# Kernel tuning notes

Measured on AMD Instinct MI355X. Metric: run time of the kernel, lower is better.

Reference implementation:

```python
import jax, jax.numpy as jnp
import numpy as np

N_NODES = 50000
N_EDGES = 640000
N_REL = 8
IN_DIM = 128
HID_DIM = 128
OUT_DIM = 64


def setup_inputs() -> dict:
    key = jax.random.key(0)
    ks = jax.random.split(key, 8)
    features = jax.random.normal(ks[0], (N_NODES, IN_DIM), dtype=jnp.float32)
    src = jax.random.randint(ks[1], (N_EDGES,), 0, N_NODES, dtype=jnp.int32)
    dst = jax.random.randint(ks[2], (N_EDGES,), 0, N_NODES, dtype=jnp.int32)
    edge_types = jax.random.randint(ks[3], (N_EDGES,), 0, N_REL, dtype=jnp.int32)
    s1 = 1.0 / np.sqrt(IN_DIM)
    s2 = 1.0 / np.sqrt(HID_DIM)
    W1 = jax.random.normal(ks[4], (N_REL, IN_DIM, HID_DIM), dtype=jnp.float32) * s1
    W1_self = jax.random.normal(ks[5], (IN_DIM, HID_DIM), dtype=jnp.float32) * s1
    b1 = jnp.zeros((HID_DIM,), dtype=jnp.float32)
    W2 = jax.random.normal(ks[6], (N_REL, HID_DIM, OUT_DIM), dtype=jnp.float32) * s2
    W2_self = jax.random.normal(ks[7], (HID_DIM, OUT_DIM), dtype=jnp.float32) * s2
    b2 = jnp.zeros((OUT_DIM,), dtype=jnp.float32)
    return {"features": features, "src": src, "dst": dst, "edge_types": edge_types,
            "W1": W1, "W1_self": W1_self, "b1": b1,
            "W2": W2, "W2_self": W2_self, "b2": b2}


def _rel_graph_conv(h, src, dst, edge_types, W, W_self, b):
    # Precompute relation-specific transforms for all nodes: [R, N, Dout]
    rel = jnp.einsum('nd,rdo->rno', h, W)
    # Gather per-edge message W[etype(e)] @ h[src(e)]: [E, Dout]
    msg = rel[edge_types, src]
    # Scatter-sum to destination nodes
    agg = jax.ops.segment_sum(msg, dst, num_segments=h.shape[0])
    # Self-loop + bias (DGL RelGraphConv defaults: self_loop=True, bias=True)
    return agg + h @ W_self + b


def reference(features, src, dst, edge_types, W1, W1_self, b1, W2, W2_self, b2):
    h = jax.nn.relu(_rel_graph_conv(features, src, dst, edge_types, W1, W1_self, b1))
    logits = _rel_graph_conv(h, src, dst, edge_types, W2, W2_self, b2)
    return logits
```

## Files before the change

kernel.cpp:

```cpp
#include <hip/hip_runtime.h>
#include <hip/hip_bf16.h>
#include <stdint.h>

#define NN 50000
#define NE 640000
#define NR 8
#define NK (NR * NN)
#define NB2 ((NK + 1023) / 1024)

typedef short bf16x8 __attribute__((ext_vector_type(8)));
typedef float f32x4  __attribute__((ext_vector_type(4)));

__device__ __forceinline__ unsigned short f2bf(float f) {
    union { float f; unsigned u; } v; v.f = f;
    unsigned r = v.u + 0x7FFF + ((v.u >> 16) & 1);
    return (unsigned short)(r >> 16);
}

__global__ void hist2_kernel(const int* __restrict__ dst, const int* __restrict__ et,
                             int* __restrict__ counts) {
    int e = blockIdx.x * 256 + threadIdx.x;
    if (e < NE) atomicAdd(&counts[et[e] * NN + dst[e]], 1);
}

__global__ __launch_bounds__(1024) void blocksum_kernel(const int* __restrict__ counts,
                                                        int* __restrict__ bsum, int n) {
    __shared__ int ws[16];
    int i = blockIdx.x * 1024 + threadIdx.x;
    int v = (i < n) ? counts[i] : 0;
    #pragma unroll
    for (int d = 32; d > 0; d >>= 1) v += __shfl_down(v, d, 64);
    int wid = threadIdx.x >> 6, lane = threadIdx.x & 63;
    if (lane == 0) ws[wid] = v;
    __syncthreads();
    if (threadIdx.x < 16) {
        int s = ws[threadIdx.x];
        #pragma unroll
        for (int d = 8; d > 0; d >>= 1) s += __shfl_down(s, d, 16);
        if (threadIdx.x == 0) bsum[blockIdx.x] = s;
    }
}

__global__ __launch_bounds__(512) void scanbase_kernel(const int* __restrict__ bsum,
                                                       int* __restrict__ base,
                                                       int* __restrict__ total, int nb) {
    __shared__ int ws[8];
    int t = threadIdx.x, lane = t & 63, wid = t >> 6;
    int v = (t < nb) ? bsum[t] : 0;
    int incl = v;
    #pragma unroll
    for (int d = 1; d < 64; d <<= 1) {
        int nv = __shfl_up(incl, d, 64);
        if (lane >= d) incl += nv;
    }
    if (lane == 63) ws[wid] = incl;
    __syncthreads();
    if (t < 8) {
        int s = ws[t], si = s;
        #pragma unroll
        for (int d = 1; d < 8; d <<= 1) {
            int nv = __shfl_up(si, d, 8);
            if (t >= d) si += nv;
        }
        ws[t] = si - s;
    }
    __syncthreads();
    int excl = ws[wid] + incl - v;
    if (t < nb) base[t] = excl;
    if (t == 511) total[0] = ws[7] + incl;
}

__global__ __launch_bounds__(1024) void scanlocal_kernel(const int* __restrict__ counts,
                                                         const int* __restrict__ base,
                                                         int* __restrict__ offsets,
                                                         int* __restrict__ cursor, int n) {
    __shared__ int ws[16];
    __shared__ int wbase[16];
    int t = threadIdx.x;
    int i = blockIdx.x * 1024 + t;
    int v = (i < n) ? counts[i] : 0;
    int lane = t & 63, wid = t >> 6;
    int incl = v;
    #pragma unroll
    for (int d = 1; d < 64; d <<= 1) {
        int nv = __shfl_up(incl, d, 64);
        if (lane >= d) incl += nv;
    }
    if (lane == 63) ws[wid] = incl;
    __syncthreads();
    if (t < 16) {
        int s = ws[t], si = s;
        #pragma unroll
        for (int d = 1; d < 16; d <<= 1) {
            int nv = __shfl_up(si, d, 16);
            if (t >= d) si += nv;
        }
        wbase[t] = si - s;
    }
    __syncthreads();
    if (i < n) {
        int excl = base[blockIdx.x] + wbase[wid] + incl - v;
        offsets[i] = excl;
        cursor[i]  = excl;
    }
}

__global__ void fill2_kernel(const int* __restrict__ src, const int* __restrict__ dst,
                             const int* __restrict__ et, int* __restrict__ cursor,
                             int* __restrict__ esrc) {
    int e = blockIdx.x * 256 + threadIdx.x;
    if (e < NE) {
        int pos = atomicAdd(&cursor[et[e] * NN + dst[e]], 1);
        esrc[pos] = src[e];
    }
}

__global__ void cvt_bf16_kernel(const float* __restrict__ in, unsigned short* __restrict__ outp,
                                int n8) {
    int i = blockIdx.x * 256 + threadIdx.x;
    if (i >= n8) return;
    const float4* pp = (const float4*)in + (size_t)i * 2;
    float4 a = pp[0], b = pp[1];
    uint4 o;
    o.x = (unsigned)f2bf(a.x) | ((unsigned)f2bf(a.y) << 16);
    o.y = (unsigned)f2bf(a.z) | ((unsigned)f2bf(a.w) << 16);
    o.z = (unsigned)f2bf(b.x) | ((unsigned)f2bf(b.y) << 16);
    o.w = (unsigned)f2bf(b.z) | ((unsigned)f2bf(b.w) << 16);
    ((uint4*)outp)[i] = o;
}

template<int DOUTV>
__global__ void prepW_kernel(const float* __restrict__ W, const float* __restrict__ Wself,
                             unsigned short* __restrict__ WT) {
    int idx = blockIdx.x * 256 + threadIdx.x;
    if (idx >= 9 * DOUTV * 128) return;
    int k = idx & 127;
    int c = idx >> 7;
    int r = c / DOUTV;
    int o = c - r * DOUTV;
    float v = (r < 8) ? W[((size_t)r * 128 + k) * DOUTV + o]
                      : Wself[(size_t)k * DOUTV + o];
    WT[idx] = f2bf(v);
}

template<int NOUT, bool RELU, bool OUTBF16>
__global__ __launch_bounds__(256) void fused_layer(
        const unsigned short* __restrict__ A,
        const unsigned short* __restrict__ WT,
        const float* __restrict__ bias,
        const int* __restrict__ off2,
        const int* __restrict__ esrc,
        void* __restrict__ outp, int M) {
    constexpr int RB = 32;
    constexpr int CW = NOUT / 4;
    constexpr int NJ = CW / 16;
    __shared__ unsigned short Asw[RB * 128];

    const int t = threadIdx.x;
    const int n0 = blockIdx.x * RB;
    const int bm = (M - n0 < RB) ? (M - n0) : RB;
    const int lane = t & 63;
    const int w = t >> 6;
    const int r15 = lane & 15;
    const int q = lane >> 4;

    const int key = t >> 3;
    const int sub = t & 7;
    const int kk = n0 + key;
    const bool kv = (kk < M);

    f32x4 acc[2][NJ] = {};

    auto do_mfma = [&](int rr) {
        #pragma unroll
        for (int ks = 0; ks < 4; ks++) {
            int c = (ks * 4 + q) ^ r15;
            bf16x8 af[2];
            #pragma unroll
            for (int i = 0; i < 2; i++)
                af[i] = *(const bf16x8*)((const char*)Asw + (i * 16 + r15) * 256 + (c << 4));
            #pragma unroll
            for (int j = 0; j < NJ; j++) {
                bf16x8 bf = *(const bf16x8*)(WT +
                    ((size_t)(rr * NOUT + w * CW + j * 16 + r15) << 7) + ks * 32 + q * 8);
                #pragma unroll
                for (int i = 0; i < 2; i++)
                    acc[i][j] = __builtin_amdgcn_mfma_f32_16x16x32_bf16(af[i], bf, acc[i][j], 0, 0, 0);
            }
        }
    };

    int e0 = kv ? off2[kk] : 0;
    int e1 = kv ? off2[kk + 1] : 0;

    #pragma unroll
    for (int kc = 0; kc < 2; kc++) {
        int g = t + kc * 256;
        int row = g >> 4, c = g & 15;
        uint4 v = make_uint4(0, 0, 0, 0);
        if (row < bm) v = *(const uint4*)(A + ((size_t)(n0 + row) << 7) + c * 8);
        *(uint4*)((char*)Asw + row * 256 + ((c ^ (row & 15)) << 4)) = v;
    }
    __syncthreads();
    do_mfma(8);

    for (int r = 0; r < 8; r++) {
        int e0n = 0, e1n = 0;
        if (r < 7 && kv) {
            e0n = off2[(r + 1) * NN + kk];
            e1n = off2[(r + 1) * NN + kk + 1];
        }

        float a[16];
        #pragma unroll
        for (int i = 0; i < 16; i++) a[i] = 0.f;
        for (int e = e0; e < e1; ++e) {
            int s = esrc[e];
            const uint4* rp = (const uint4*)((const unsigned*)A + ((size_t)s << 6) + sub * 8);
            #pragma unroll
            for (int u4 = 0; u4 < 2; ++u4) {
                uint4 v = rp[u4];
                unsigned uu[4] = {v.x, v.y, v.z, v.w};
                #pragma unroll
                for (int j = 0; j < 4; ++j) {
                    a[u4 * 8 + j * 2 + 0] += __uint_as_float(uu[j] << 16);
                    a[u4 * 8 + j * 2 + 1] += __uint_as_float(uu[j] & 0xffff0000u);
                }
            }
        }
        __syncthreads();

        #pragma unroll
        for (int c4 = 0; c4 < 2; ++c4) {
            uint4 pv;
            pv.x = (unsigned)f2bf(a[c4 * 8 + 0]) | ((unsigned)f2bf(a[c4 * 8 + 1]) << 16);
            pv.y = (unsigned)f2bf(a[c4 * 8 + 2]) | ((unsigned)f2bf(a[c4 * 8 + 3]) << 16);
            pv.z = (unsigned)f2bf(a[c4 * 8 + 4]) | ((unsigned)f2bf(a[c4 * 8 + 5]) << 16);
            pv.w = (unsigned)f2bf(a[c4 * 8 + 6]) | ((unsigned)f2bf(a[c4 * 8 + 7]) << 16);
            int c = sub * 2 + c4;
            *(uint4*)((char*)Asw + key * 256 + ((c ^ (key & 15)) << 4)) = pv;
        }
        __syncthreads();

        do_mfma(r);
        e0 = e0n; e1 = e1n;
    }

    #pragma unroll
    for (int j = 0; j < NJ; j++) {
        int col = w * CW + j * 16 + r15;
        float bv = bias[col];
        #pragma unroll
        for (int i = 0; i < 2; i++) {
            #pragma unroll
            for (int reg = 0; reg < 4; reg++) {
                int m = n0 + i * 16 + q * 4 + reg;
                if (m < M) {
                    float v = acc[i][j][reg] + bv;
                    if (RELU) v = fmaxf(v, 0.f);
                    if (OUTBF16)
                        ((unsigned short*)outp)[(size_t)m * NOUT + col] = f2bf(v);
                    else
                        ((float*)outp)[(size_t)m * NOUT + col] = v;
                }
            }
        }
    }
}

extern "C" void kernel_launch(void* const* d_in, const int* in_sizes, int n_in,
                              void* d_out, int out_size, void* d_ws, size_t ws_size,
                              hipStream_t stream) {
    const float* X   = (const float*)d_in[0];
    const int*   src = (const int*)d_in[1];
    const int*   dst = (const int*)d_in[2];
    const int*   et  = (const int*)d_in[3];
    const float* W1  = (const float*)d_in[4];
    const float* W1s = (const float*)d_in[5];
    const float* b1  = (const float*)d_in[6];
    const float* W2  = (const float*)d_in[7];
    const float* W2s = (const float*)d_in[8];
    const float* b2  = (const float*)d_in[9];
    float* out = (float*)d_out;

    char* p = (char*)d_ws;
    unsigned short* Xbf = (unsigned short*)p; p += (size_t)NN * 128 * 2;
    unsigned short* hbf = (unsigned short*)p; p += (size_t)NN * 128 * 2;
    unsigned short* W1T = (unsigned short*)p; p += (size_t)9 * 128 * 128 * 2;
    unsigned short* W2T = (unsigned short*)p; p += (size_t)9 * 64 * 128 * 2;
    int* counts2 = (int*)p; p += (size_t)NK * 4;
    int* off2    = (int*)p; p += (size_t)(NK + 4) * 4;
    int* cursor2 = (int*)p; p += (size_t)NK * 4;
    int* esrc    = (int*)p; p += (size_t)NE * 4;
    int* bsum    = (int*)p; p += 512 * 4;
    int* bbase   = (int*)p; p += 512 * 4;

    hipMemsetAsync(counts2, 0, (size_t)NK * sizeof(int), stream);
    hist2_kernel<<<(NE + 255) / 256, 256, 0, stream>>>(dst, et, counts2);
    blocksum_kernel<<<NB2, 1024, 0, stream>>>(counts2, bsum, NK);
    scanbase_kernel<<<1, 512, 0, stream>>>(bsum, bbase, &off2[NK], NB2);
    scanlocal_kernel<<<NB2, 1024, 0, stream>>>(counts2, bbase, off2, cursor2, NK);
    fill2_kernel<<<(NE + 255) / 256, 256, 0, stream>>>(src, dst, et, cursor2, esrc);

    cvt_bf16_kernel<<<(NN * 128 / 8 + 255) / 256, 256, 0, stream>>>(X, Xbf, NN * 128 / 8);
    prepW_kernel<128><<<(9 * 128 * 128 + 255) / 256, 256, 0, stream>>>(W1, W1s, W1T);
    prepW_kernel<64><<<(9 * 64 * 128 + 255) / 256, 256, 0, stream>>>(W2, W2s, W2T);

    const int nblk = (NN + 31) / 32;

    fused_layer<128, true, true><<<nblk, 256, 0, stream>>>(
        Xbf, W1T, b1, off2, esrc, hbf, NN);
    fused_layer<64, false, false><<<nblk, 256, 0, stream>>>(
        hbf, W2T, b2, off2, esrc, out, NN);
}
```

Before: 332.7 us.

## Double node tile to 64 rows and gather two relations per pass

```diff
diff --git a/kernel.cpp b/kernel.cpp
--- a/kernel.cpp
+++ b/kernel.cpp
@@ -151,99 +151,124 @@
         const int* __restrict__ off2,
         const int* __restrict__ esrc,
         void* __restrict__ outp, int M) {
-    constexpr int RB = 32;
     constexpr int CW = NOUT / 4;
     constexpr int NJ = CW / 16;
-    __shared__ unsigned short Asw[RB * 128];
+    __shared__ unsigned short Asw[2][64 * 128];
 
     const int t = threadIdx.x;
-    const int n0 = blockIdx.x * RB;
-    const int bm = (M - n0 < RB) ? (M - n0) : RB;
+    const int n0 = blockIdx.x * 64;
+    const int bm = (M - n0 < 64) ? (M - n0) : 64;
     const int lane = t & 63;
     const int w = t >> 6;
     const int r15 = lane & 15;
     const int q = lane >> 4;
 
-    const int key = t >> 3;
-    const int sub = t & 7;
+    const int key = t >> 2;
+    const int sub = t & 3;
     const int kk = n0 + key;
     const bool kv = (kk < M);
 
-    f32x4 acc[2][NJ] = {};
-
-    auto do_mfma = [&](int rr) {
+    f32x4 acc[4][NJ] = {};
+
+    auto do_mfma = [&](int rr, const unsigned short* buf) {
         #pragma unroll
         for (int ks = 0; ks < 4; ks++) {
             int c = (ks * 4 + q) ^ r15;
-            bf16x8 af[2];
+            bf16x8 af[4];
             #pragma unroll
-            for (int i = 0; i < 2; i++)
-                af[i] = *(const bf16x8*)((const char*)Asw + (i * 16 + r15) * 256 + (c << 4));
+            for (int i = 0; i < 4; i++)
+                af[i] = *(const bf16x8*)((const char*)buf + (i * 16 + r15) * 256 + (c << 4));
             #pragma unroll
             for (int j = 0; j < NJ; j++) {
                 bf16x8 bf = *(const bf16x8*)(WT +
                     ((size_t)(rr * NOUT + w * CW + j * 16 + r15) << 7) + ks * 32 + q * 8);
                 #pragma unroll
-                for (int i = 0; i < 2; i++)
+                for (int i = 0; i < 4; i++)
                     acc[i][j] = __builtin_amdgcn_mfma_f32_16x16x32_bf16(af[i], bf, acc[i][j], 0, 0, 0);
             }
         }
     };
 
-    int e0 = kv ? off2[kk] : 0;
-    int e1 = kv ? off2[kk + 1] : 0;
-
-    #pragma unroll
-    for (int kc = 0; kc < 2; kc++) {
-        int g = t + kc * 256;
-        int row = g >> 4, c = g & 15;
-        uint4 v = make_uint4(0, 0, 0, 0);
-        if (row < bm) v = *(const uint4*)(A + ((size_t)(n0 + row) << 7) + c * 8);
-        *(uint4*)((char*)Asw + row * 256 + ((c ^ (row & 15)) << 4)) = v;
-    }
-    __syncthreads();
-    do_mfma(8);
-
-    for (int r = 0; r < 8; r++) {
-        int e0n = 0, e1n = 0;
-        if (r < 7 && kv) {
-            e0n = off2[(r + 1) * NN + kk];
-            e1n = off2[(r + 1) * NN + kk + 1];
-        }
-
-        float a[16];
-        #pragma unroll
-        for (int i = 0; i < 16; i++) a[i] = 0.f;
-        for (int e = e0; e < e1; ++e) {
-            int s = esrc[e];
-            const uint4* rp = (const uint4*)((const unsigned*)A + ((size_t)s << 6) + sub * 8);
-            #pragma unroll
-            for (int u4 = 0; u4 < 2; ++u4) {
-                uint4 v = rp[u4];
-                unsigned uu[4] = {v.x, v.y, v.z, v.w};
-                #pragma unroll
-                for (int j = 0; j < 4; ++j) {
-                    a[u4 * 8 + j * 2 + 0] += __uint_as_float(uu[j] << 16);
-                    a[u4 * 8 + j * 2 + 1] += __uint_as_float(uu[j] & 0xffff0000u);
-                }
-            }
-        }
-        __syncthreads();
-
-        #pragma unroll
-        for (int c4 = 0; c4 < 2; ++c4) {
+    auto do_pack = [&](const float* a, unsigned short* buf) {
+        #pragma unroll
+        for (int c4 = 0; c4 < 4; ++c4) {
             uint4 pv;
             pv.x = (unsigned)f2bf(a[c4 * 8 + 0]) | ((unsigned)f2bf(a[c4 * 8 + 1]) << 16);
             pv.y = (unsigned)f2bf(a[c4 * 8 + 2]) | ((unsigned)f2bf(a[c4 * 8 + 3]) << 16);
             pv.z = (unsigned)f2bf(a[c4 * 8 + 4]) | ((unsigned)f2bf(a[c4 * 8 + 5]) << 16);
             pv.w = (unsigned)f2bf(a[c4 * 8 + 6]) | ((unsigned)f2bf(a[c4 * 8 + 7]) << 16);
-            int c = sub * 2 + c4;
-            *(uint4*)((char*)Asw + key * 256 + ((c ^ (key & 15)) << 4)) = pv;
-        }
+            int c = sub * 4 + c4;
+            *(uint4*)((char*)buf + key * 256 + ((c ^ (key & 15)) << 4)) = pv;
+        }
+    };
+
+    int a0 = 0, a1 = 0, b0 = 0, b1 = 0;
+    if (kv) {
+        a0 = off2[kk];            a1 = off2[kk + 1];
+        b0 = off2[NN + kk];       b1 = off2[NN + kk + 1];
+    }
+
+    #pragma unroll
+    for (int kc = 0; kc < 4; kc++) {
+        int g = t + kc * 256;
+        int row = g >> 4, c = g & 15;
+        uint4 v = make_uint4(0, 0, 0, 0);
+        if (row < bm) v = *(const uint4*)(A + ((size_t)(n0 + row) << 7) + c * 8);
+        *(uint4*)((char*)Asw[0] + row * 256 + ((c ^ (row & 15)) << 4)) = v;
+    }
+    __syncthreads();
+    do_mfma(8, Asw[0]);
+
+    for (int p = 0; p < 4; p++) {
+        int r = 2 * p;
+        int na0 = 0, na1 = 0, nb0 = 0, nb1 = 0;
+        if (p < 3 && kv) {
+            na0 = off2[(r + 2) * NN + kk]; na1 = off2[(r + 2) * NN + kk + 1];
+            nb0 = off2[(r + 3) * NN + kk]; nb1 = off2[(r + 3) * NN + kk + 1];
+        }
+
+        float aA[32], aB[32];
+        #pragma unroll
+        for (int i = 0; i < 32; i++) { aA[i] = 0.f; aB[i] = 0.f; }
+        int ea = a0, eb = b0;
+        while (ea < a1 || eb < b1) {
+            bool va = ea < a1, vb = eb < b1;
+            int sa = va ? esrc[ea] : 0;
+            int sb = vb ? esrc[eb] : 0;
+            const uint4* rpa = (const uint4*)((const unsigned*)A + ((size_t)sa << 6) + sub * 16);
+            const uint4* rpb = (const uint4*)((const unsigned*)A + ((size_t)sb << 6) + sub * 16);
+            uint4 wa0 = rpa[0], wa1 = rpa[1], wa2 = rpa[2], wa3 = rpa[3];
+            uint4 wb0 = rpb[0], wb1 = rpb[1], wb2 = rpb[2], wb3 = rpb[3];
+            if (va) {
+                unsigned uu[16] = {wa0.x, wa0.y, wa0.z, wa0.w, wa1.x, wa1.y, wa1.z, wa1.w,
+                                   wa2.x, wa2.y, wa2.z, wa2.w, wa3.x, wa3.y, wa3.z, wa3.w};
+                #pragma unroll
+                for (int j = 0; j < 16; ++j) {
+                    aA[j * 2 + 0] += __uint_as_float(uu[j] << 16);
+                    aA[j * 2 + 1] += __uint_as_float(uu[j] & 0xffff0000u);
+                }
+            }
+            if (vb) {
+                unsigned uu[16] = {wb0.x, wb0.y, wb0.z, wb0.w, wb1.x, wb1.y, wb1.z, wb1.w,
+                                   wb2.x, wb2.y, wb2.z, wb2.w, wb3.x, wb3.y, wb3.z, wb3.w};
+                #pragma unroll
+                for (int j = 0; j < 16; ++j) {
+                    aB[j * 2 + 0] += __uint_as_float(uu[j] << 16);
+                    aB[j * 2 + 1] += __uint_as_float(uu[j] & 0xffff0000u);
+                }
+            }
+            ++ea; ++eb;
+        }
+
         __syncthreads();
-
-        do_mfma(r);
-        e0 = e0n; e1 = e1n;
+        do_pack(aA, Asw[0]);
+        do_pack(aB, Asw[1]);
+        __syncthreads();
+
+        do_mfma(r, Asw[0]);
+        do_mfma(r + 1, Asw[1]);
+
+        a0 = na0; a1 = na1; b0 = nb0; b1 = nb1;
     }
 
     #pragma unroll
@@ -251,7 +276,7 @@
         int col = w * CW + j * 16 + r15;
         float bv = bias[col];
         #pragma unroll
-        for (int i = 0; i < 2; i++) {
+        for (int i = 0; i < 4; i++) {
             #pragma unroll
             for (int reg = 0; reg < 4; reg++) {
                 int m = n0 + i * 16 + q * 4 + reg;
@@ -306,7 +331,7 @@
     prepW_kernel<128><<<(9 * 128 * 128 + 255) / 256, 256, 0, stream>>>(W1, W1s, W1T);
     prepW_kernel<64><<<(9 * 64 * 128 + 255) / 256, 256, 0, stream>>>(W2, W2s, W2T);
 
-    const int nblk = (NN + 31) / 32;
+    const int nblk = (NN + 63) / 64;
 
     fused_layer<128, true, true><<<nblk, 256, 0, stream>>>(
         Xbf, W1T, b1, off2, esrc, hbf, NN);
```

New measurement: 350.3 us. +5.3%, slower.
